# Optimization experiments

Hardware: AMD Instinct MI355X
Metric: run time of the kernel (lower is better)

## Reference

```python
import jax, jax.numpy as jnp
import numpy as np
from functools import partial

L, B, E, H, NL = 512, 16, 768, 12, 12
D = E // H  # head dim = 64
FF = 4 * E
LN_EPS = 1e-5


def gelu_new(x):
    # HF openai-gpt ACT_FNS['gelu'] (tanh approximation)
    c = np.sqrt(2.0 / np.pi).astype(np.float32)
    return 0.5 * x * (1.0 + jnp.tanh(c * (x + 0.044715 * x * x * x)))


def layer_norm(x, g, b):
    mu = jnp.mean(x, axis=-1, keepdims=True)
    var = jnp.mean(jnp.square(x - mu), axis=-1, keepdims=True)
    return (x - mu) * jax.lax.rsqrt(var + LN_EPS) * g + b


def setup_inputs() -> dict:
    key = jax.random.key(0)
    ks = jax.random.split(key, 8)
    s = 0.02
    x = jax.random.normal(ks[0], (L, B, E), dtype=jnp.float32)
    custom_mask = jnp.ones((B, L), dtype=jnp.float32)
    pos_emb = s * jax.random.normal(ks[1], (L, E), dtype=jnp.float32)
    # stacked per-layer params (leading axis = layer)
    params = {
        'c_attn_w': s * jax.random.normal(ks[2], (NL, E, 3 * E), dtype=jnp.float32),
        'c_attn_b': jnp.zeros((NL, 3 * E), dtype=jnp.float32),
        'attn_proj_w': s * jax.random.normal(ks[3], (NL, E, E), dtype=jnp.float32),
        'attn_proj_b': jnp.zeros((NL, E), dtype=jnp.float32),
        'ln1_g': jnp.ones((NL, E), dtype=jnp.float32),
        'ln1_b': jnp.zeros((NL, E), dtype=jnp.float32),
        'c_fc_w': s * jax.random.normal(ks[4], (NL, E, FF), dtype=jnp.float32),
        'c_fc_b': jnp.zeros((NL, FF), dtype=jnp.float32),
        'mlp_proj_w': s * jax.random.normal(ks[5], (NL, FF, E), dtype=jnp.float32),
        'mlp_proj_b': jnp.zeros((NL, E), dtype=jnp.float32),
        'ln2_g': jnp.ones((NL, E), dtype=jnp.float32),
        'ln2_b': jnp.zeros((NL, E), dtype=jnp.float32),
    }
    return {'x': x, 'custom_mask': custom_mask, 'pos_emb': pos_emb, **params}


def _gpt_forward(x, custom_mask, pos_emb, c_attn_w, c_attn_b, attn_proj_w,
                 attn_proj_b, ln1_g, ln1_b, c_fc_w, c_fc_b, mlp_proj_w,
                 mlp_proj_b, ln2_g, ln2_b):
    Lx, Bx, Ex = x.shape
    h = x.transpose(1, 0, 2) + pos_emb[None, :Lx]  # (B, L, E); dropout = eval identity
    # additive padding mask: (1 - m) * finfo.min, broadcast over heads/queries
    add_mask = (1.0 - custom_mask)[:, None, None, :] * jnp.finfo(jnp.float32).min
    causal = jnp.tril(jnp.ones((Lx, Lx), dtype=jnp.float32))  # bias buffer b

    def block(h, p):
        (caw, cab, apw, apb, g1, b1, fw, fb, pw, pb, g2, b2) = p
        qkv = h @ caw + cab                              # (B, L, 3E)
        q, k, v = jnp.split(qkv, 3, axis=-1)
        q = q.reshape(Bx, Lx, H, D).transpose(0, 2, 1, 3)  # (B, H, L, D)
        k = k.reshape(Bx, Lx, H, D).transpose(0, 2, 1, 3)
        v = v.reshape(Bx, Lx, H, D).transpose(0, 2, 1, 3)
        w = jnp.einsum('bhqd,bhkd->bhqk', q, k) / np.float32(np.sqrt(D))
        w = w * causal + (-10000.0) * (1.0 - causal)     # causal bias masking
        w = w + add_mask
        a = jax.nn.softmax(w, axis=-1)
        o = jnp.einsum('bhqk,bhkd->bhqd', a, v)          # (B, H, L, D)
        o = o.transpose(0, 2, 1, 3).reshape(Bx, Lx, Ex)
        a_out = o @ apw + apb
        n = layer_norm(h + a_out, g1, b1)
        m = gelu_new(n @ fw + fb) @ pw + pb
        h2 = layer_norm(n + m, g2, b2)
        return h2, None

    params = (c_attn_w, c_attn_b, attn_proj_w, attn_proj_b, ln1_g, ln1_b,
              c_fc_w, c_fc_b, mlp_proj_w, mlp_proj_b, ln2_g, ln2_b)
    h, _ = jax.lax.scan(block, h, params)
    return h.transpose(1, 0, 2)  # back to (L, B, E)


def reference(x, custom_mask, pos_emb, c_attn_w, c_attn_b, attn_proj_w,
              attn_proj_b, ln1_g, ln1_b, c_fc_w, c_fc_b, mlp_proj_w,
              mlp_proj_b, ln2_g, ln2_b):
    return _gpt_forward(x, custom_mask, pos_emb, c_attn_w, c_attn_b,
                        attn_proj_w, attn_proj_b, ln1_g, ln1_b, c_fc_w,
                        c_fc_b, mlp_proj_w, mlp_proj_b, ln2_g, ln2_b)
```

## Files before the change

kernel.cpp:

```cpp
#include <hip/hip_runtime.h>
#include <cstdint>
#include <cstddef>


#define LSEQ 512
#define NBATCH 16
#define EDIM 768
#define NHEAD 12
#define NLAYER 12

typedef __attribute__((ext_vector_type(8))) short short8;
typedef __attribute__((ext_vector_type(4))) short short4v;
typedef __attribute__((ext_vector_type(4))) float f32x4;

__device__ __forceinline__ short f2bf(float f) {
  union { float f; unsigned u; } x; x.f = f;
  return (short)((x.u + 0x7FFFu + ((x.u >> 16) & 1u)) >> 16);
}
__device__ __forceinline__ float bf2f(short s) {
  union { unsigned u; float f; } x; x.u = ((unsigned)(unsigned short)s) << 16;
  return x.f;
}

__device__ __forceinline__ void gload_lds16(const void* g, void* l) {
  __builtin_amdgcn_global_load_lds(
      (__attribute__((address_space(1))) void*)(void*)g,
      (__attribute__((address_space(3))) void*)l, 16, 0, 0);
}

__global__ __launch_bounds__(256) void wt_transpose(const float* __restrict__ W,
                                                    short* __restrict__ Wt,
                                                    int K, int N) {
  __shared__ float tile[32][33];
  const int n0 = blockIdx.x * 32, k0 = blockIdx.y * 32;
  const size_t lo = (size_t)blockIdx.z * K * N;
  const float* Ws = W + lo;
  short* Wd = Wt + lo;
  const int tx = threadIdx.x & 31, ty = threadIdx.x >> 5;
#pragma unroll
  for (int i = 0; i < 4; ++i)
    tile[ty + i * 8][tx] = Ws[(size_t)(k0 + ty + i * 8) * N + n0 + tx];
  __syncthreads();
#pragma unroll
  for (int i = 0; i < 4; ++i)
    Wd[(size_t)(n0 + ty + i * 8) * K + k0 + tx] = f2bf(tile[tx][ty + i * 8]);
}

__global__ __launch_bounds__(256) void embed_k(const float* __restrict__ x,
                                               const float* __restrict__ pos,
                                               float* __restrict__ h,
                                               short* __restrict__ hbf) {
  const int row = blockIdx.x;
  const int b = row >> 9, lp = row & 511;
  const int t = threadIdx.x;
#pragma unroll
  for (int i = 0; i < 3; ++i) {
    const int e = t + i * 256;
    float v = x[(size_t)(lp * 16 + b) * 768 + e] + pos[(size_t)lp * 768 + e];
    h[(size_t)row * 768 + e] = v;
    hbf[(size_t)row * 768 + e] = f2bf(v);
  }
}

__global__ __launch_bounds__(256) void final_k(const float* __restrict__ h,
                                               float* __restrict__ out) {
  const int row = blockIdx.x;
  const int lp = row >> 4, b = row & 15;
  const int t = threadIdx.x;
#pragma unroll
  for (int i = 0; i < 3; ++i) {
    const int e = t + i * 256;
    out[(size_t)row * 768 + e] = h[(size_t)(b * 512 + lp) * 768 + e];
  }
}

__global__ __launch_bounds__(256) void ln_fused(const float* __restrict__ A,
                                                const short* __restrict__ B,
                                                const float* __restrict__ g,
                                                const float* __restrict__ be,
                                                float* __restrict__ outf,
                                                short* __restrict__ outb) {
  const int row = blockIdx.x * 4 + (threadIdx.x >> 6);
  const int l = threadIdx.x & 63;
  const size_t base = (size_t)row * 768;
  float v[12];
  float s1 = 0.f, s2 = 0.f;
#pragma unroll
  for (int j = 0; j < 3; ++j) {
    const int e = j * 256 + l * 4;
    f32x4 a = *(const f32x4*)&A[base + e];
    short4v b = *(const short4v*)&B[base + e];
#pragma unroll
    for (int q = 0; q < 4; ++q) {
      float x = a[q] + bf2f(b[q]);
      v[j * 4 + q] = x; s1 += x; s2 += x * x;
    }
  }
#pragma unroll
  for (int m = 1; m < 64; m <<= 1) {
    s1 += __shfl_xor(s1, m);
    s2 += __shfl_xor(s2, m);
  }
  const float mu = s1 * (1.f / 768.f);
  const float rs = rsqrtf(s2 * (1.f / 768.f) - mu * mu + 1e-5f);
#pragma unroll
  for (int j = 0; j < 3; ++j) {
    const int e = j * 256 + l * 4;
    f32x4 gv = *(const f32x4*)&g[e];
    f32x4 bv = *(const f32x4*)&be[e];
    f32x4 of; short4v ob;
#pragma unroll
    for (int q = 0; q < 4; ++q) {
      float o = (v[j * 4 + q] - mu) * rs * gv[q] + bv[q];
      of[q] = o; ob[q] = f2bf(o);
    }
    *(f32x4*)&outf[base + e] = of;
    *(short4v*)&outb[base + e] = ob;
  }
}

template <int EPI>
__global__ __launch_bounds__(512) void gemm512(const short* __restrict__ A,
                                               const short* __restrict__ Bt,
                                               const float* __restrict__ bias,
                                               short* __restrict__ C,
                                               int N, int K) {
  constexpr int BK = 64;
  __shared__ alignas(16) short Alds[128 * BK];
  __shared__ alignas(16) short Blds[256 * BK];
  const int t = threadIdx.x;
  const int w = t >> 6, l = t & 63;
  const int wr = w >> 2, wc = w & 3;
  const int l15 = l & 15, lhi = l >> 4;
  const int rowA0 = blockIdx.x * 128;
  const int rowB0 = blockIdx.y * 256;

  f32x4 acc[4][4];
#pragma unroll
  for (int mi = 0; mi < 4; ++mi)
#pragma unroll
    for (int ni = 0; ni < 4; ++ni) acc[mi][ni] = (f32x4){0.f, 0.f, 0.f, 0.f};

  const int srl = w * 8 + (l >> 3);
  const int ss = l & 7;

  const short* aptr[2];
#pragma unroll
  for (int i = 0; i < 2; ++i) {
    const int r = i * 64 + srl;
    aptr[i] = A + (size_t)(rowA0 + r) * K + ((ss ^ (r & 7)) << 3);
  }
  const short* bptr[4];
#pragma unroll
  for (int i = 0; i < 4; ++i) {
    const int r = i * 64 + srl;
    bptr[i] = Bt + (size_t)(rowB0 + r) * K + ((ss ^ (r & 7)) << 3);
  }

  for (int kt = 0; kt < K; kt += BK) {
#pragma unroll
    for (int i = 0; i < 2; ++i) {
      gload_lds16(aptr[i], &Alds[(i * 64 + w * 8) * BK]);
      aptr[i] += BK;
    }
#pragma unroll
    for (int i = 0; i < 4; ++i) {
      gload_lds16(bptr[i], &Blds[(i * 64 + w * 8) * BK]);
      bptr[i] += BK;
    }
    __syncthreads();
    short8 af[4][2], bfr[4][2];
#pragma unroll
    for (int mi = 0; mi < 4; ++mi) {
      const int r = wr * 64 + mi * 16 + l15;
#pragma unroll
      for (int kc = 0; kc < 2; ++kc)
        af[mi][kc] = *(const short8*)
            &Alds[r * BK + ((((kc << 2) | lhi) ^ (r & 7)) << 3)];
    }
#pragma unroll
    for (int ni = 0; ni < 4; ++ni) {
      const int r = wc * 64 + ni * 16 + l15;
#pragma unroll
      for (int kc = 0; kc < 2; ++kc)
        bfr[ni][kc] = *(const short8*)
            &Blds[r * BK + ((((kc << 2) | lhi) ^ (r & 7)) << 3)];
    }
#pragma unroll
    for (int mi = 0; mi < 4; ++mi)
#pragma unroll
      for (int ni = 0; ni < 4; ++ni)
#pragma unroll
        for (int kc = 0; kc < 2; ++kc)
          acc[mi][ni] = __builtin_amdgcn_mfma_f32_16x16x32_bf16(
              af[mi][kc], bfr[ni][kc], acc[mi][ni], 0, 0, 0);
    __syncthreads();
  }

  float bv[4];
#pragma unroll
  for (int ni = 0; ni < 4; ++ni) bv[ni] = bias[rowB0 + wc * 64 + ni * 16 + l15];
#pragma unroll
  for (int mi = 0; mi < 4; ++mi) {
#pragma unroll
    for (int ni = 0; ni < 4; ++ni) {
      const int col = rowB0 + wc * 64 + ni * 16 + l15;
#pragma unroll
      for (int i = 0; i < 4; ++i) {
        const int row = rowA0 + wr * 64 + mi * 16 + lhi * 4 + i;
        float v = acc[mi][ni][i] + bv[ni];
        if constexpr (EPI == 1) {
          C[(size_t)row * N + col] = f2bf(v);
        } else {
          float pz = v * fmaf(0.044715f, v * v, 1.0f);
          float e = __expf(-1.5957691216057308f * pz);
          float r = __builtin_amdgcn_rcpf(1.0f + e);
          C[(size_t)row * N + col] = f2bf(v * r);
        }
      }
    }
  }
}

template <int TN, int EPI>
__global__ __launch_bounds__(256) void gemm_bt(const short* __restrict__ A,
                                               const short* __restrict__ Bt,
                                               const float* __restrict__ bias,
                                               void* __restrict__ C,
                                               int N, int K) {
  constexpr int BK = 64;
  __shared__ alignas(16) short Alds[128 * BK];
  __shared__ alignas(16) short Blds[TN * BK];
  const int t = threadIdx.x;
  const int w = t >> 6, l = t & 63;
  constexpr int WR = (TN == 128) ? 2 : 4;
  constexpr int WC = (TN == 128) ? 2 : 1;
  constexpr int WM = 128 / WR;
  constexpr int MI = WM / 16;
  constexpr int NI = (TN / WC) / 16;
  const int wr = (WC == 2) ? (w >> 1) : w;
  const int wc = (WC == 2) ? (w & 1) : 0;
  const int l15 = l & 15, lhi = l >> 4;
  const int rowA0 = blockIdx.x * 128;
  const int rowB0 = blockIdx.y * TN;
  f32x4 acc[MI][NI];
#pragma unroll
  for (int mi = 0; mi < MI; ++mi)
#pragma unroll
    for (int ni = 0; ni < NI; ++ni) acc[mi][ni] = (f32x4){0.f, 0.f, 0.f, 0.f};

  const int srl = l >> 3;
  const int ss = l & 7;

  for (int kt = 0; kt < K; kt += BK) {
#pragma unroll
    for (int i = 0; i < 4; ++i) {
      const int r = i * 32 + w * 8 + srl;
      gload_lds16(A + (size_t)(rowA0 + r) * K + kt + ((ss ^ (r & 7)) << 3),
                  &Alds[i * 2048 + w * 512]);
    }
#pragma unroll
    for (int i = 0; i < TN / 32; ++i) {
      const int r = i * 32 + w * 8 + srl;
      gload_lds16(Bt + (size_t)(rowB0 + r) * K + kt + ((ss ^ (r & 7)) << 3),
                  &Blds[i * 2048 + w * 512]);
    }
    __syncthreads();
    short8 af[MI][2], bfr[NI][2];
#pragma unroll
    for (int mi = 0; mi < MI; ++mi) {
      const int r = wr * WM + mi * 16 + l15;
#pragma unroll
      for (int kc = 0; kc < 2; ++kc)
        af[mi][kc] = *(const short8*)
            &Alds[r * 64 + ((((kc << 2) | lhi) ^ (r & 7)) << 3)];
    }
#pragma unroll
    for (int ni = 0; ni < NI; ++ni) {
      const int r = wc * 64 + ni * 16 + l15;
#pragma unroll
      for (int kc = 0; kc < 2; ++kc)
        bfr[ni][kc] = *(const short8*)
            &Blds[r * 64 + ((((kc << 2) | lhi) ^ (r & 7)) << 3)];
    }
#pragma unroll
    for (int mi = 0; mi < MI; ++mi)
#pragma unroll
      for (int ni = 0; ni < NI; ++ni)
#pragma unroll
        for (int kc = 0; kc < 2; ++kc)
          acc[mi][ni] = __builtin_amdgcn_mfma_f32_16x16x32_bf16(
              af[mi][kc], bfr[ni][kc], acc[mi][ni], 0, 0, 0);
    __syncthreads();
  }

  float bv[NI];
#pragma unroll
  for (int ni = 0; ni < NI; ++ni) bv[ni] = bias[rowB0 + wc * 64 + ni * 16 + l15];
#pragma unroll
  for (int mi = 0; mi < MI; ++mi) {
#pragma unroll
    for (int ni = 0; ni < NI; ++ni) {
      const int col = rowB0 + wc * 64 + ni * 16 + l15;
#pragma unroll
      for (int i = 0; i < 4; ++i) {
        const int row = rowA0 + wr * WM + mi * 16 + lhi * 4 + i;
        float v = acc[mi][ni][i] + bv[ni];
        if constexpr (EPI == 0) {
          ((float*)C)[(size_t)row * N + col] = v;
        } else {
          ((short*)C)[(size_t)row * N + col] = f2bf(v);
        }
      }
    }
  }
}

__global__ __launch_bounds__(256) void attn_k(const short* __restrict__ qkv,
                                              const float* __restrict__ mask,
                                              short* __restrict__ o) {
  const int qb = blockIdx.x;
  const int hh = blockIdx.y;
  const int b = blockIdx.z;
  const int t = threadIdx.x, w = t >> 6, l = t & 63;
  const int l15 = l & 15, lhi = l >> 4;
  __shared__ alignas(16) short Klds[64 * 64];
  __shared__ alignas(16) short Vlds[64 * 64];
  __shared__ alignas(16) short Plds[4][16 * 72];

  short8 qa[2];
  {
    const size_t base =
        (size_t)(b * LSEQ + qb * 64 + w * 16 + l15) * 2304 + hh * 64;
    qa[0] = *(const short8*)&qkv[base + lhi * 8];
    qa[1] = *(const short8*)&qkv[base + 32 + lhi * 8];
  }
  float mrow[4] = {-1e30f, -1e30f, -1e30f, -1e30f};
  float lrow[4] = {0.f, 0.f, 0.f, 0.f};
  const f32x4 zero4 = {0.f, 0.f, 0.f, 0.f};
  f32x4 oacc[4];
#pragma unroll
  for (int nt = 0; nt < 4; ++nt) oacc[nt] = zero4;

  const int nkt = qb + 1;
  for (int kt = 0; kt < nkt; ++kt) {
    __syncthreads();
    {
      const int kr = t >> 2, cc = (t & 3) * 16;
      const size_t grow = (size_t)(b * LSEQ + kt * 64 + kr) * 2304 + hh * 64;
      short8 k0 = *(const short8*)&qkv[grow + 768 + cc];
      short8 k1 = *(const short8*)&qkv[grow + 768 + cc + 8];
      short8 v0 = *(const short8*)&qkv[grow + 1536 + cc];
      short8 v1 = *(const short8*)&qkv[grow + 1536 + cc + 8];
      const int sw = (kr & 7) << 4;
      *(short8*)((char*)Klds + ((kr * 128 + cc * 2) ^ sw)) = k0;
      *(short8*)((char*)Klds + ((kr * 128 + cc * 2 + 16) ^ sw)) = k1;
#pragma unroll
      for (int e = 0; e < 8; ++e) {
        const int n0 = cc + e, n1 = cc + 8 + e;
        ((short*)Vlds)[((n0 * 128 + kr * 2) ^ ((n0 & 7) << 4)) >> 1] = v0[e];
        ((short*)Vlds)[((n1 * 128 + kr * 2) ^ ((n1 & 7) << 4)) >> 1] = v1[e];
      }
    }
    __syncthreads();

    f32x4 s[4];
#pragma unroll
    for (int jt = 0; jt < 4; ++jt) {
      f32x4 z = zero4;
#pragma unroll
      for (int kc = 0; kc < 2; ++kc) {
        const int rowk = jt * 16 + l15;
        short8 kb = *(const short8*)((char*)Klds +
                     ((rowk * 128 + kc * 64 + lhi * 16) ^ ((rowk & 7) << 4)));
        z = __builtin_amdgcn_mfma_f32_16x16x32_bf16(qa[kc], kb, z, 0, 0, 0);
      }
      s[jt] = z;
    }

    float addm[4];
#pragma unroll
    for (int jt = 0; jt < 4; ++jt)
      addm[jt] = (1.0f - mask[b * LSEQ + kt * 64 + jt * 16 + l15]) *
                 -3.402823466e38f;
#pragma unroll
    for (int jt = 0; jt < 4; ++jt) {
      const int colg = kt * 64 + jt * 16 + l15;
#pragma unroll
      for (int i = 0; i < 4; ++i) {
        const int rowg = qb * 64 + w * 16 + lhi * 4 + i;
        float sv = s[jt][i] * 0.125f;
        if (colg > rowg) sv = -10000.0f;
        s[jt][i] = sv + addm[jt];
      }
    }

    float mnew[4], sc[4];
#pragma unroll
    for (int i = 0; i < 4; ++i) {
      float tm = fmaxf(fmaxf(s[0][i], s[1][i]), fmaxf(s[2][i], s[3][i]));
#pragma unroll
      for (int mm = 1; mm < 16; mm <<= 1) tm = fmaxf(tm, __shfl_xor(tm, mm));
      mnew[i] = fmaxf(mrow[i], tm);
      sc[i] = __expf(mrow[i] - mnew[i]);
      mrow[i] = mnew[i];
    }
#pragma unroll
    for (int i = 0; i < 4; ++i) {
      float ts = 0.f;
#pragma unroll
      for (int jt = 0; jt < 4; ++jt) {
        float p = __expf(s[jt][i] - mnew[i]);
        s[jt][i] = p;
        ts += p;
      }
#pragma unroll
      for (int mm = 1; mm < 16; mm <<= 1) ts += __shfl_xor(ts, mm);
      lrow[i] = lrow[i] * sc[i] + ts;
      oacc[0][i] *= sc[i]; oacc[1][i] *= sc[i];
      oacc[2][i] *= sc[i]; oacc[3][i] *= sc[i];
    }

    short* Pw = &Plds[w][0];
#pragma unroll
    for (int jt = 0; jt < 4; ++jt)
#pragma unroll
      for (int i = 0; i < 4; ++i)
        Pw[(lhi * 4 + i) * 72 + jt * 16 + l15] = f2bf(s[jt][i]);
    __syncthreads();
    short8 pa[2];
#pragma unroll
    for (int kc = 0; kc < 2; ++kc)
      pa[kc] = *(const short8*)&Pw[l15 * 72 + kc * 32 + lhi * 8];

#pragma unroll
    for (int nt = 0; nt < 4; ++nt) {
#pragma unroll
      for (int kc = 0; kc < 2; ++kc) {
        const int rown = nt * 16 + l15;
        short8 vb = *(const short8*)((char*)Vlds +
                     ((rown * 128 + kc * 64 + lhi * 16) ^ ((rown & 7) << 4)));
        oacc[nt] = __builtin_amdgcn_mfma_f32_16x16x32_bf16(pa[kc], vb,
                                                           oacc[nt], 0, 0, 0);
      }
    }
  }

#pragma unroll
  for (int i = 0; i < 4; ++i) {
    const size_t row = (size_t)(b * LSEQ + qb * 64 + w * 16 + lhi * 4 + i);
    const float inv = 1.0f / lrow[i];
#pragma unroll
    for (int nt = 0; nt < 4; ++nt)
      o[row * 768 + hh * 64 + nt * 16 + l15] = f2bf(oacc[nt][i] * inv);
  }
}

extern "C" void kernel_launch(void* const* d_in, const int* in_sizes, int n_in,
                              void* d_out, int out_size, void* d_ws,
                              size_t ws_size, hipStream_t stream) {
  const float* x    = (const float*)d_in[0];
  const float* mask = (const float*)d_in[1];
  const float* pos  = (const float*)d_in[2];
  const float* caw  = (const float*)d_in[3];
  const float* cab  = (const float*)d_in[4];
  const float* apw  = (const float*)d_in[5];
  const float* apb  = (const float*)d_in[6];
  const float* g1   = (const float*)d_in[7];
  const float* b1   = (const float*)d_in[8];
  const float* fw   = (const float*)d_in[9];
  const float* fb   = (const float*)d_in[10];
  const float* pw   = (const float*)d_in[11];
  const float* pb   = (const float*)d_in[12];
  const float* g2   = (const float*)d_in[13];
  const float* b2   = (const float*)d_in[14];

  char* ws = (char*)d_ws;
  size_t off = 0;
  auto alloc = [&](size_t bytes) {
    size_t o = off;
    off += (bytes + 255) & ~(size_t)255;
    return o;
  };
  float* h    = (float*)(ws + alloc(8192ull * 768 * 4));
  short* hbf  = (short*)(ws + alloc(8192ull * 768 * 2));
  float* nrm  = (float*)(ws + alloc(8192ull * 768 * 4));
  short* nbf  = (short*)(ws + alloc(8192ull * 768 * 2));
  short* qkvb = (short*)(ws + alloc(8192ull * 2304 * 2));
  short* obf  = (short*)(ws + alloc(8192ull * 768 * 2));
  short* aout = (short*)(ws + alloc(8192ull * 768 * 2));
  short* gbf  = (short*)(ws + alloc(8192ull * 3072 * 2));
  short* wt_attn = (short*)(ws + alloc(12ull * 768 * 2304 * 2));
  short* wt_proj = (short*)(ws + alloc(12ull * 768 * 768 * 2));
  short* wt_fc   = (short*)(ws + alloc(12ull * 768 * 3072 * 2));
  short* wt_mlp  = (short*)(ws + alloc(12ull * 3072 * 768 * 2));
  (void)ws_size; (void)in_sizes; (void)n_in; (void)out_size;

  wt_transpose<<<dim3(2304 / 32, 768 / 32, 12), 256, 0, stream>>>(caw, wt_attn, 768, 2304);
  wt_transpose<<<dim3(768 / 32, 768 / 32, 12), 256, 0, stream>>>(apw, wt_proj, 768, 768);
  wt_transpose<<<dim3(3072 / 32, 768 / 32, 12), 256, 0, stream>>>(fw, wt_fc, 768, 3072);
  wt_transpose<<<dim3(768 / 32, 3072 / 32, 12), 256, 0, stream>>>(pw, wt_mlp, 3072, 768);

  embed_k<<<8192, 256, 0, stream>>>(x, pos, h, hbf);

  for (int L = 0; L < 12; ++L) {
    gemm512<1><<<dim3(64, 9), 512, 0, stream>>>(
        hbf, wt_attn + (size_t)L * 2304 * 768, cab + (size_t)L * 2304, qkvb, 2304, 768);
    attn_k<<<dim3(8, 12, 16), 256, 0, stream>>>(qkvb, mask, obf);
    gemm_bt<64, 1><<<dim3(64, 12), 256, 0, stream>>>(
        obf, wt_proj + (size_t)L * 768 * 768, apb + (size_t)L * 768, aout, 768, 768);
    ln_fused<<<2048, 256, 0, stream>>>(h, aout, g1 + (size_t)L * 768,
                                       b1 + (size_t)L * 768, nrm, nbf);
    gemm512<2><<<dim3(64, 12), 512, 0, stream>>>(
        nbf, wt_fc + (size_t)L * 768 * 3072, fb + (size_t)L * 3072, gbf, 3072, 768);
    gemm_bt<64, 1><<<dim3(64, 12), 256, 0, stream>>>(
        gbf, wt_mlp + (size_t)L * 3072 * 768, pb + (size_t)L * 768, aout, 768, 3072);
    ln_fused<<<2048, 256, 0, stream>>>(nrm, aout, g2 + (size_t)L * 768,
                                       b2 + (size_t)L * 768, h, hbf);
  }

  final_k<<<8192, 256, 0, stream>>>(h, (float*)d_out);
}
```

Before: 3.364 ms.

## Split-K the N=768 projection GEMMs and sum partials in layer norm

The two N=768 GEMMs (attention output projection and MLP down-projection) move from 128x64 tiles to 128x128 tiles and split K in two via blockIdx.z. Each half writes its own bf16 partial buffer, and the following layer-norm kernel adds both partials. Larger tiles give more data reuse per block while split-K keeps the grid at 768 blocks. The cost is an extra partial-output write and read, plus an additional bf16 rounding of the partial sums.

```diff
diff --git a/kernel.cpp b/kernel.cpp
--- a/kernel.cpp
+++ b/kernel.cpp
@@ -75,7 +75,8 @@
 }
 
 __global__ __launch_bounds__(256) void ln_fused(const float* __restrict__ A,
-                                                const short* __restrict__ B,
+                                                const short* __restrict__ B0,
+                                                const short* __restrict__ B1,
                                                 const float* __restrict__ g,
                                                 const float* __restrict__ be,
                                                 float* __restrict__ outf,
@@ -89,10 +90,11 @@
   for (int j = 0; j < 3; ++j) {
     const int e = j * 256 + l * 4;
     f32x4 a = *(const f32x4*)&A[base + e];
-    short4v b = *(const short4v*)&B[base + e];
+    short4v b0 = *(const short4v*)&B0[base + e];
+    short4v b1 = *(const short4v*)&B1[base + e];
 #pragma unroll
     for (int q = 0; q < 4; ++q) {
-      float x = a[q] + bf2f(b[q]);
+      float x = a[q] + bf2f(b0[q]) + bf2f(b1[q]);
       v[j * 4 + q] = x; s1 += x; s2 += x * x;
     }
   }
@@ -222,61 +224,62 @@
   }
 }
 
-template <int TN, int EPI>
-__global__ __launch_bounds__(256) void gemm_bt(const short* __restrict__ A,
+__global__ __launch_bounds__(256) void gemm_pk(const short* __restrict__ A,
                                                const short* __restrict__ Bt,
                                                const float* __restrict__ bias,
-                                               void* __restrict__ C,
-                                               int N, int K) {
+                                               short* __restrict__ C,
+                                               int N, int Kfull) {
   constexpr int BK = 64;
   __shared__ alignas(16) short Alds[128 * BK];
-  __shared__ alignas(16) short Blds[TN * BK];
+  __shared__ alignas(16) short Blds[128 * BK];
   const int t = threadIdx.x;
   const int w = t >> 6, l = t & 63;
-  constexpr int WR = (TN == 128) ? 2 : 4;
-  constexpr int WC = (TN == 128) ? 2 : 1;
-  constexpr int WM = 128 / WR;
-  constexpr int MI = WM / 16;
-  constexpr int NI = (TN / WC) / 16;
-  const int wr = (WC == 2) ? (w >> 1) : w;
-  const int wc = (WC == 2) ? (w & 1) : 0;
+  const int wr = w >> 1, wc = w & 1;
   const int l15 = l & 15, lhi = l >> 4;
   const int rowA0 = blockIdx.x * 128;
-  const int rowB0 = blockIdx.y * TN;
-  f32x4 acc[MI][NI];
-#pragma unroll
-  for (int mi = 0; mi < MI; ++mi)
-#pragma unroll
-    for (int ni = 0; ni < NI; ++ni) acc[mi][ni] = (f32x4){0.f, 0.f, 0.f, 0.f};
+  const int rowB0 = blockIdx.y * 128;
+  const int z = blockIdx.z;
+  const int Ks = Kfull >> 1;
+  const int koff = z * Ks;
+  short* Cp = C + (size_t)z * 8192 * N;
+
+  f32x4 acc[4][4];
+#pragma unroll
+  for (int mi = 0; mi < 4; ++mi)
+#pragma unroll
+    for (int ni = 0; ni < 4; ++ni) acc[mi][ni] = (f32x4){0.f, 0.f, 0.f, 0.f};
 
   const int srl = l >> 3;
   const int ss = l & 7;
 
-  for (int kt = 0; kt < K; kt += BK) {
+  const short* aptr[4];
+  const short* bptr[4];
+#pragma unroll
+  for (int i = 0; i < 4; ++i) {
+    const int r = i * 32 + w * 8 + srl;
+    aptr[i] = A + (size_t)(rowA0 + r) * Kfull + koff + ((ss ^ (r & 7)) << 3);
+    bptr[i] = Bt + (size_t)(rowB0 + r) * Kfull + koff + ((ss ^ (r & 7)) << 3);
+  }
+
+  for (int kt = 0; kt < Ks; kt += BK) {
 #pragma unroll
     for (int i = 0; i < 4; ++i) {
-      const int r = i * 32 + w * 8 + srl;
-      gload_lds16(A + (size_t)(rowA0 + r) * K + kt + ((ss ^ (r & 7)) << 3),
-                  &Alds[i * 2048 + w * 512]);
-    }
-#pragma unroll
-    for (int i = 0; i < TN / 32; ++i) {
-      const int r = i * 32 + w * 8 + srl;
-      gload_lds16(Bt + (size_t)(rowB0 + r) * K + kt + ((ss ^ (r & 7)) << 3),
-                  &Blds[i * 2048 + w * 512]);
-    }
-    __syncthreads();
-    short8 af[MI][2], bfr[NI][2];
-#pragma unroll
-    for (int mi = 0; mi < MI; ++mi) {
-      const int r = wr * WM + mi * 16 + l15;
+      gload_lds16(aptr[i], &Alds[i * 2048 + w * 512]);
+      gload_lds16(bptr[i], &Blds[i * 2048 + w * 512]);
+      aptr[i] += BK; bptr[i] += BK;
+    }
+    __syncthreads();
+    short8 af[4][2], bfr[4][2];
+#pragma unroll
+    for (int mi = 0; mi < 4; ++mi) {
+      const int r = wr * 64 + mi * 16 + l15;
 #pragma unroll
       for (int kc = 0; kc < 2; ++kc)
         af[mi][kc] = *(const short8*)
             &Alds[r * 64 + ((((kc << 2) | lhi) ^ (r & 7)) << 3)];
     }
 #pragma unroll
-    for (int ni = 0; ni < NI; ++ni) {
+    for (int ni = 0; ni < 4; ++ni) {
       const int r = wc * 64 + ni * 16 + l15;
 #pragma unroll
       for (int kc = 0; kc < 2; ++kc)
@@ -284,9 +287,9 @@
             &Blds[r * 64 + ((((kc << 2) | lhi) ^ (r & 7)) << 3)];
     }
 #pragma unroll
-    for (int mi = 0; mi < MI; ++mi)
-#pragma unroll
-      for (int ni = 0; ni < NI; ++ni)
+    for (int mi = 0; mi < 4; ++mi)
+#pragma unroll
+      for (int ni = 0; ni < 4; ++ni)
 #pragma unroll
         for (int kc = 0; kc < 2; ++kc)
           acc[mi][ni] = __builtin_amdgcn_mfma_f32_16x16x32_bf16(
@@ -294,23 +297,19 @@
     __syncthreads();
   }
 
-  float bv[NI];
-#pragma unroll
-  for (int ni = 0; ni < NI; ++ni) bv[ni] = bias[rowB0 + wc * 64 + ni * 16 + l15];
-#pragma unroll
-  for (int mi = 0; mi < MI; ++mi) {
-#pragma unroll
-    for (int ni = 0; ni < NI; ++ni) {
+  float bv[4];
+#pragma unroll
+  for (int ni = 0; ni < 4; ++ni)
+    bv[ni] = (z == 0) ? bias[rowB0 + wc * 64 + ni * 16 + l15] : 0.f;
+#pragma unroll
+  for (int mi = 0; mi < 4; ++mi) {
+#pragma unroll
+    for (int ni = 0; ni < 4; ++ni) {
       const int col = rowB0 + wc * 64 + ni * 16 + l15;
 #pragma unroll
       for (int i = 0; i < 4; ++i) {
-        const int row = rowA0 + wr * WM + mi * 16 + lhi * 4 + i;
-        float v = acc[mi][ni][i] + bv[ni];
-        if constexpr (EPI == 0) {
-          ((float*)C)[(size_t)row * N + col] = v;
-        } else {
-          ((short*)C)[(size_t)row * N + col] = f2bf(v);
-        }
+        const int row = rowA0 + wr * 64 + mi * 16 + lhi * 4 + i;
+        Cp[(size_t)row * N + col] = f2bf(acc[mi][ni][i] + bv[ni]);
       }
     }
   }
@@ -488,12 +487,13 @@
   short* nbf  = (short*)(ws + alloc(8192ull * 768 * 2));
   short* qkvb = (short*)(ws + alloc(8192ull * 2304 * 2));
   short* obf  = (short*)(ws + alloc(8192ull * 768 * 2));
-  short* aout = (short*)(ws + alloc(8192ull * 768 * 2));
+  short* aout = (short*)(ws + alloc(2ull * 8192 * 768 * 2));
   short* gbf  = (short*)(ws + alloc(8192ull * 3072 * 2));
   short* wt_attn = (short*)(ws + alloc(12ull * 768 * 2304 * 2));
   short* wt_proj = (short*)(ws + alloc(12ull * 768 * 768 * 2));
   short* wt_fc   = (short*)(ws + alloc(12ull * 768 * 3072 * 2));
   short* wt_mlp  = (short*)(ws + alloc(12ull * 3072 * 768 * 2));
+  short* aout1 = aout + 8192ull * 768;
   (void)ws_size; (void)in_sizes; (void)n_in; (void)out_size;
 
   wt_transpose<<<dim3(2304 / 32, 768 / 32, 12), 256, 0, stream>>>(caw, wt_attn, 768, 2304);
@@ -507,15 +507,15 @@
     gemm512<1><<<dim3(64, 9), 512, 0, stream>>>(
         hbf, wt_attn + (size_t)L * 2304 * 768, cab + (size_t)L * 2304, qkvb, 2304, 768);
     attn_k<<<dim3(8, 12, 16), 256, 0, stream>>>(qkvb, mask, obf);
-    gemm_bt<64, 1><<<dim3(64, 12), 256, 0, stream>>>(
+    gemm_pk<<<dim3(64, 6, 2), 256, 0, stream>>>(
         obf, wt_proj + (size_t)L * 768 * 768, apb + (size_t)L * 768, aout, 768, 768);
-    ln_fused<<<2048, 256, 0, stream>>>(h, aout, g1 + (size_t)L * 768,
+    ln_fused<<<2048, 256, 0, stream>>>(h, aout, aout1, g1 + (size_t)L * 768,
                                        b1 + (size_t)L * 768, nrm, nbf);
     gemm512<2><<<dim3(64, 12), 512, 0, stream>>>(
         nbf, wt_fc + (size_t)L * 768 * 3072, fb + (size_t)L * 3072, gbf, 3072, 768);
-    gemm_bt<64, 1><<<dim3(64, 12), 256, 0, stream>>>(
+    gemm_pk<<<dim3(64, 6, 2), 256, 0, stream>>>(
         gbf, wt_mlp + (size_t)L * 3072 * 768, pb + (size_t)L * 768, aout, 768, 3072);
-    ln_fused<<<2048, 256, 0, stream>>>(nrm, aout, g2 + (size_t)L * 768,
+    ln_fused<<<2048, 256, 0, stream>>>(nrm, aout, aout1, g2 + (size_t)L * 768,
                                        b2 + (size_t)L * 768, h, hbf);
   }
 
```

After: 3.265 ms. 1.03x faster.
